# Performance work log

Measured on AMD Instinct MI355X. Metric: run time of the kernel, lower is better.

## Reference

```python
import jax, jax.numpy as jnp
import numpy as np

NUM_NODES = 262144        # 1024 graphs x 256 nodes
NODES_PER_GRAPH = 256
NUM_GRAPHS = NUM_NODES // NODES_PER_GRAPH
NUM_EDGES = 2097152       # avg degree 8
NUM_FEATURES = 9
NUM_STATIONS = 8


def setup_inputs() -> dict:
    key = jax.random.key(0)
    ks = jax.random.split(key, 12)
    # edges constrained within each graph so batched-graph semantics hold
    src_local = jax.random.randint(ks[0], (NUM_EDGES,), 0, NODES_PER_GRAPH)
    dst_local = jax.random.randint(ks[1], (NUM_EDGES,), 0, NODES_PER_GRAPH)
    graph_of_edge = jax.random.randint(ks[2], (NUM_EDGES,), 0, NUM_GRAPHS)
    offset = graph_of_edge * NODES_PER_GRAPH
    edge_index = jnp.stack([src_local + offset, dst_local + offset]).astype(jnp.int64)
    station_ids = jnp.array([0, 37, 73, 110, 146, 183, 219, 255], dtype=jnp.int64)
    s = lambda k, shape, fan_in: jax.random.normal(k, shape, jnp.float32) / np.sqrt(fan_in)
    return {
        "x": jax.random.normal(ks[3], (NUM_NODES, NUM_FEATURES), jnp.float32),
        "edge_index": edge_index,
        "station_ids": station_ids,
        "W1": s(ks[4], (NUM_FEATURES, 32), NUM_FEATURES),
        "b1": jnp.zeros((32,), jnp.float32),
        "W2": s(ks[5], (32, 64), 32),
        "b2": jnp.zeros((64,), jnp.float32),
        "fc1_W": s(ks[6], (128, 64), 128),
        "fc1_b": jnp.zeros((64,), jnp.float32),
        "fc2_W": s(ks[7], (64, 1), 64),
        "fc2_b": jnp.zeros((1,), jnp.float32),
    }


def _gcn_conv(x, W, b, src, dst, n_nodes):
    """PyG GCNConv: add self-loops, symmetric normalization, linear first."""
    h = x @ W                                              # [N, C_out]
    # degree includes the self-loop (+1), counted on target nodes
    deg = jnp.zeros((n_nodes,), h.dtype).at[dst].add(1.0) + 1.0
    dinv = jax.lax.rsqrt(deg)                              # deg >= 1, safe
    norm = dinv[src] * dinv[dst]                           # [E]
    out = jnp.zeros_like(h).at[dst].add(norm[:, None] * h[src])
    out = out + (dinv * dinv)[:, None] * h                 # self-loop term
    return out + b


def reference(x, edge_index, station_ids, W1, b1, W2, b2, fc1_W, fc1_b, fc2_W, fc2_b):
    n = x.shape[0]
    src, dst = edge_index[0], edge_index[1]
    h = jax.nn.relu(_gcn_conv(x, W1, b1, src, dst, n))     # [N, 32]
    h = jax.nn.relu(_gcn_conv(h, W2, b2, src, dst, n))     # [N, 64]
    # global mean pool per graph (batch = node_idx // NODES_PER_GRAPH)
    batch = jnp.arange(n) // NODES_PER_GRAPH
    sums = jax.ops.segment_sum(h, batch, num_segments=NUM_GRAPHS)
    counts = jax.ops.segment_sum(jnp.ones((n,), h.dtype), batch, num_segments=NUM_GRAPHS)
    global_ctx = sums / counts[:, None]                    # [B, 64]
    # per-station gather-MLP, vectorized over stations
    idx = jnp.arange(NUM_GRAPHS)[:, None] * NODES_PER_GRAPH + station_ids[None, :]  # [B, S]
    station_emb = h[idx]                                   # [B, S, 64]
    ctx = jnp.broadcast_to(global_ctx[:, None, :], station_emb.shape)
    combined = jnp.concatenate([station_emb, ctx], axis=-1)  # [B, S, 128]
    q = jax.nn.relu(combined @ fc1_W + fc1_b) @ fc2_W + fc2_b  # [B, S, 1]
    return q[..., 0]                                       # [B, S]
```

## Files before the change

kernel.cpp:

```cpp
#include <hip/hip_runtime.h>
#include <hip/hip_bf16.h>


#define NNODES 262144
#define NPG 256
#define NGRAPHS 1024
#define NEDGES 2097152
#define NFEAT 9
#define ECAP2 2560
#define T_EDGES 8192
#define NTILES (NEDGES / T_EDGES)
#define TPB 512
#define NBLK 256

typedef __hip_bfloat16 bf16;
typedef short short8 __attribute__((ext_vector_type(8)));
typedef float f32x4 __attribute__((ext_vector_type(4)));

__device__ __forceinline__ float bfbits(unsigned short u) { return __uint_as_float(((unsigned)u) << 16); }
__device__ __forceinline__ unsigned short f2bbits(float v) { bf16 b = __float2bfloat16(v); return *(unsigned short*)&b; }


__global__ void __launch_bounds__(1024) k_gsort(const int* __restrict__ src,
                                                const int* __restrict__ dst,
                                                int* __restrict__ gcur,
                                                unsigned short* __restrict__ gout) {
    __shared__ unsigned short edg[T_EDGES];
    __shared__ unsigned short pay[T_EDGES];
    __shared__ int cnt[NGRAPHS];
    __shared__ int goff[NGRAPHS];
    int t = threadIdx.x;
    int base = blockIdx.x * T_EDGES;
    cnt[t] = 0;
    __syncthreads();
    const int4* s4 = (const int4*)(src + base);
    const int4* d4 = (const int4*)(dst + base);
#pragma unroll
    for (int k = 0; k < T_EDGES / 4096; ++k) {
        int idx = k * 1024 + t;
        int4 dv = d4[idx];
        int4 sv = s4[idx];
        int i0 = idx * 4;
        edg[i0]     = (unsigned short)(dv.x >> 8);
        edg[i0 + 1] = (unsigned short)(dv.y >> 8);
        edg[i0 + 2] = (unsigned short)(dv.z >> 8);
        edg[i0 + 3] = (unsigned short)(dv.w >> 8);
        pay[i0]     = (unsigned short)(((dv.x & 255) << 8) | (sv.x & 255));
        pay[i0 + 1] = (unsigned short)(((dv.y & 255) << 8) | (sv.y & 255));
        pay[i0 + 2] = (unsigned short)(((dv.z & 255) << 8) | (sv.z & 255));
        pay[i0 + 3] = (unsigned short)(((dv.w & 255) << 8) | (sv.w & 255));
        atomicAdd(&cnt[dv.x >> 8], 1);
        atomicAdd(&cnt[dv.y >> 8], 1);
        atomicAdd(&cnt[dv.z >> 8], 1);
        atomicAdd(&cnt[dv.w >> 8], 1);
    }
    __syncthreads();
    {
        int c = cnt[t];
        goff[t] = c ? atomicAdd(&gcur[t * 16], c) : 0;
        cnt[t] = 0;
    }
    __syncthreads();
#pragma unroll
    for (int k = 0; k < T_EDGES / 1024; ++k) {
        int i = k * 1024 + t;
        int g = edg[i];
        int pos = atomicAdd(&cnt[g], 1);
        int off = goff[g] + pos;
        if (off < ECAP2) gout[(size_t)g * ECAP2 + off] = pay[i];
    }
}


__global__ void __launch_bounds__(TPB) k_fused(
    const float* __restrict__ x, const int* __restrict__ station_ids,
    const float* __restrict__ W1, const float* __restrict__ b1,
    const float* __restrict__ W2, const float* __restrict__ b2,
    const float* __restrict__ fc1W, const float* __restrict__ fc1b,
    const float* __restrict__ fc2W, const float* __restrict__ fc2b,
    const int* __restrict__ gcnt, const unsigned short* __restrict__ gedges,
    float* __restrict__ out) {

    __shared__ __align__(16) unsigned char Ms[65536];
    __shared__ __align__(16) unsigned char BufA[17024];
    __shared__ __align__(16) unsigned char BufB[17024];
    __shared__ __align__(16) unsigned char BufC[19456];
    __shared__ __align__(16) unsigned short fc1s16[8192];
    __shared__ __align__(16) unsigned short W2Ts[64 * 40];
    __shared__ float W1s[288];
    __shared__ float dinvs[256];
    __shared__ unsigned short Rl[260];
    __shared__ unsigned char El[ECAP2];
    __shared__ unsigned int sru[512];
    __shared__ float sts[512];
    __shared__ float meanf[64];
    __shared__ float poolf[64];
    __shared__ unsigned char stmap[256];
    __shared__ float b1s[32], b2s[64], fc1bs[64], fc2ws[64];
    __shared__ int stids[8];
    __shared__ float fc2bv;

    int t = threadIdx.x;
    int lane = t & 63, wvid = t >> 6;
    int m = lane & 15, quad = lane >> 4;

    float* xsf = (float*)BufC;
    unsigned short* EPa = (unsigned short*)(BufC + 9216);
    unsigned short* G1T = (unsigned short*)BufA;
    unsigned short* H1T = (unsigned short*)BufB;
    unsigned short* S2 = (unsigned short*)BufC;

    for (int i = t; i < NFEAT * 32; i += TPB) W1s[i] = W1[i];
    for (int i = t; i < 2048; i += TPB)
        W2Ts[(i >> 5) * 40 + (i & 31)] = f2bbits(W2[(i & 31) * 64 + (i >> 5)]);
    for (int i = t; i < 8192; i += TPB) fc1s16[i] = f2bbits(fc1W[i]);
    if (t < 32) b1s[t] = b1[t];
    if (t < 64) { b2s[t] = b2[t]; fc1bs[t] = fc1b[t]; fc2ws[t] = fc2W[t]; }
    if (t < 8) stids[t] = station_ids[t];
    if (t == 0) fc2bv = fc2b[0];
    if (t < 256) stmap[t] = 255;
    __syncthreads();
    if (t < 8) stmap[stids[t] & 255] = (unsigned char)t;

    for (int g = blockIdx.x; g < NGRAPHS; g += NBLK) {
        int nbase = g * NPG;

        int ecnt = min(gcnt[g * 16], ECAP2);
        {
            const uint4* gev = (const uint4*)(gedges + (size_t)g * ECAP2);
            uint4* epv = (uint4*)EPa;
            for (int i = t; i < ECAP2 / 8; i += TPB) epv[i] = gev[i];
        }
        const float* xg = x + (size_t)nbase * NFEAT;
        for (int i = t; i < NPG * NFEAT; i += TPB) xsf[i] = xg[i];
        if (t < 64) poolf[t] = 0.f;
        if (t < 256) sru[t] = 0u;
        {
            uint4* mz = (uint4*)Ms;
            uint4 z = {0u, 0u, 0u, 0u};
            for (int i = t; i < 4096; i += TPB) mz[i] = z;
        }
        __syncthreads();

        for (int i = t; i < ecnt; i += TPB) atomicAdd(&sru[EPa[i] >> 8], 1u);
        __syncthreads();

        if (wvid == 0) {
            int b0 = sru[lane * 4], b1v = sru[lane * 4 + 1], b2v = sru[lane * 4 + 2], b3 = sru[lane * 4 + 3];
            int s = b0 + b1v + b2v + b3;
            int inc = s;
            for (int off = 1; off < 64; off <<= 1) {
                int y = __shfl_up(inc, off);
                if (lane >= off) inc += y;
            }
            int run = inc - s;
            Rl[lane * 4] = (unsigned short)run; sru[256 + lane * 4] = run;
            dinvs[lane * 4] = rsqrtf((float)(b0 + 1)); run += b0;
            Rl[lane * 4 + 1] = (unsigned short)run; sru[257 + lane * 4] = run;
            dinvs[lane * 4 + 1] = rsqrtf((float)(b1v + 1)); run += b1v;
            Rl[lane * 4 + 2] = (unsigned short)run; sru[258 + lane * 4] = run;
            dinvs[lane * 4 + 2] = rsqrtf((float)(b2v + 1)); run += b2v;
            Rl[lane * 4 + 3] = (unsigned short)run; sru[259 + lane * 4] = run;
            dinvs[lane * 4 + 3] = rsqrtf((float)(b3 + 1));
            if (lane == 63) Rl[256] = (unsigned short)inc;
        }
        __syncthreads();

        for (int i = t; i < ecnt; i += TPB) {
            unsigned short v = EPa[i];
            unsigned p = atomicAdd(&sru[256 + (v >> 8)], 1u);
            if (p < ECAP2) El[p] = (unsigned char)(v & 255);
        }
        __syncthreads();

        if (t < 256) {
            int dl = t >> 1, q = t & 1;
            int d = dl;
            float did = dinvs[d];
            if ((d >> 7) == q)
                *(unsigned short*)(Ms + dl * 512 + (((d >> 3) ^ (d & 15)) * 16) + (d & 7) * 2)
                    = f2bbits(did * did);
            int r0 = Rl[d], r1 = Rl[d + 1];
            for (int e = r0; e < r1; ++e) {
                int s = El[e];
                if ((s >> 7) == q) {
                    unsigned short* p =
                        (unsigned short*)(Ms + dl * 512 + (((s >> 3) ^ (d & 15)) * 16) + (s & 7) * 2);
                    *p = f2bbits(bfbits(*p) + did * dinvs[s]);
                }
            }
        } else {
            int n = t - 256;
            float xv[NFEAT];
#pragma unroll
            for (int k = 0; k < NFEAT; k++) xv[k] = xsf[n * NFEAT + k];
#pragma unroll 4
            for (int c = 0; c < 32; c++) {
                float acc = 0.f;
#pragma unroll
                for (int k = 0; k < NFEAT; k++) acc += xv[k] * W1s[k * 32 + c];
                G1T[c * 266 + n] = f2bbits(acc);
            }
        }
        __syncthreads();

        {
            f32x4 acc[2] = {};
            for (int kt = 0; kt < 8; ++kt) {
                short8 af = *(const short8*)(Ms + (wvid * 16 + m) * 512 + (((kt * 4 + quad) ^ m) * 16));
                short8 bf0 = *(const short8*)(BufA + (size_t)m * 532 + kt * 64 + quad * 16);
                short8 bf1 = *(const short8*)(BufA + (size_t)(16 + m) * 532 + kt * 64 + quad * 16);
                acc[0] = __builtin_amdgcn_mfma_f32_16x16x32_bf16(af, bf0, acc[0], 0, 0, 0);
                acc[1] = __builtin_amdgcn_mfma_f32_16x16x32_bf16(af, bf1, acc[1], 0, 0, 0);
            }
#pragma unroll
            for (int ni = 0; ni < 2; ++ni) {
                int ch = ni * 16 + m;
                float bb = b1s[ch];
#pragma unroll
                for (int r = 0; r < 4; ++r) {
                    int node = wvid * 16 + quad * 4 + r;
                    H1T[ch * 266 + node] = f2bbits(fmaxf(acc[ni][r] + bb, 0.f));
                }
            }
        }
        __syncthreads();

        {
            uint4* mz = (uint4*)Ms;
            uint4 z = {0u, 0u, 0u, 0u};
            for (int i = t; i < 4096; i += TPB) mz[i] = z;
        }
        __syncthreads();
        {
            int dl = t >> 2, q = t & 3;
            int d = 128 + dl;
            float did = dinvs[d];
            if (((d & 255) >> 6) == q) {
                int sd = d & 255;
                *(unsigned short*)(Ms + dl * 512 + (((sd >> 3) ^ (d & 15)) * 16) + (sd & 7) * 2)
                    = f2bbits(did * did);
            }
            int r0 = Rl[d], r1 = Rl[d + 1];
            for (int e = r0; e < r1; ++e) {
                int s = El[e];
                if ((s >> 6) == q) {
                    unsigned short* p =
                        (unsigned short*)(Ms + dl * 512 + (((s >> 3) ^ (d & 15)) * 16) + (s & 7) * 2);
                    *p = f2bbits(bfbits(*p) + did * dinvs[s]);
                }
            }
        }
        __syncthreads();

        {
            f32x4 acc[2] = {};
            for (int kt = 0; kt < 8; ++kt) {
                short8 af = *(const short8*)(Ms + (wvid * 16 + m) * 512 + (((kt * 4 + quad) ^ m) * 16));
                short8 bf0 = *(const short8*)(BufA + (size_t)m * 532 + kt * 64 + quad * 16);
                short8 bf1 = *(const short8*)(BufA + (size_t)(16 + m) * 532 + kt * 64 + quad * 16);
                acc[0] = __builtin_amdgcn_mfma_f32_16x16x32_bf16(af, bf0, acc[0], 0, 0, 0);
                acc[1] = __builtin_amdgcn_mfma_f32_16x16x32_bf16(af, bf1, acc[1], 0, 0, 0);
            }
#pragma unroll
            for (int ni = 0; ni < 2; ++ni) {
                int ch = ni * 16 + m;
                float bb = b1s[ch];
#pragma unroll
                for (int r = 0; r < 4; ++r) {
                    int node = 128 + wvid * 16 + quad * 4 + r;
                    H1T[ch * 266 + node] = f2bbits(fmaxf(acc[ni][r] + bb, 0.f));
                }
            }
        }
        __syncthreads();

        {
            f32x4 acc[2] = {};
            for (int kt = 0; kt < 8; ++kt) {
                short8 af = *(const short8*)(Ms + (wvid * 16 + m) * 512 + (((kt * 4 + quad) ^ m) * 16));
                short8 bf0 = *(const short8*)(BufB + (size_t)m * 532 + kt * 64 + quad * 16);
                short8 bf1 = *(const short8*)(BufB + (size_t)(16 + m) * 532 + kt * 64 + quad * 16);
                acc[0] = __builtin_amdgcn_mfma_f32_16x16x32_bf16(af, bf0, acc[0], 0, 0, 0);
                acc[1] = __builtin_amdgcn_mfma_f32_16x16x32_bf16(af, bf1, acc[1], 0, 0, 0);
            }
#pragma unroll
            for (int ni = 0; ni < 2; ++ni) {
                int ch = ni * 16 + m;
#pragma unroll
                for (int r = 0; r < 4; ++r) {
                    int node = 128 + wvid * 16 + quad * 4 + r;
                    S2[node * 38 + ch] = f2bbits(acc[ni][r]);
                }
            }
        }
        __syncthreads();

        {
            uint4* mz = (uint4*)Ms;
            uint4 z = {0u, 0u, 0u, 0u};
            for (int i = t; i < 4096; i += TPB) mz[i] = z;
        }
        __syncthreads();
        {
            int dl = t >> 2, q = t & 3;
            int d = dl;
            float did = dinvs[d];
            if ((d >> 6) == q)
                *(unsigned short*)(Ms + dl * 512 + (((d >> 3) ^ (d & 15)) * 16) + (d & 7) * 2)
                    = f2bbits(did * did);
            int r0 = Rl[d], r1 = Rl[d + 1];
            for (int e = r0; e < r1; ++e) {
                int s = El[e];
                if ((s >> 6) == q) {
                    unsigned short* p =
                        (unsigned short*)(Ms + dl * 512 + (((s >> 3) ^ (d & 15)) * 16) + (s & 7) * 2);
                    *p = f2bbits(bfbits(*p) + did * dinvs[s]);
                }
            }
        }
        __syncthreads();

        {
            f32x4 acc[2] = {};
            for (int kt = 0; kt < 8; ++kt) {
                short8 af = *(const short8*)(Ms + (wvid * 16 + m) * 512 + (((kt * 4 + quad) ^ m) * 16));
                short8 bf0 = *(const short8*)(BufB + (size_t)m * 532 + kt * 64 + quad * 16);
                short8 bf1 = *(const short8*)(BufB + (size_t)(16 + m) * 532 + kt * 64 + quad * 16);
                acc[0] = __builtin_amdgcn_mfma_f32_16x16x32_bf16(af, bf0, acc[0], 0, 0, 0);
                acc[1] = __builtin_amdgcn_mfma_f32_16x16x32_bf16(af, bf1, acc[1], 0, 0, 0);
            }
#pragma unroll
            for (int ni = 0; ni < 2; ++ni) {
                int ch = ni * 16 + m;
#pragma unroll
                for (int r = 0; r < 4; ++r) {
                    int node = wvid * 16 + quad * 4 + r;
                    S2[node * 38 + ch] = f2bbits(acc[ni][r]);
                }
            }
        }
        __syncthreads();

        {
#pragma unroll
            for (int mi = 0; mi < 2; ++mi) {
                int mt = wvid * 2 + mi;
                short8 af = *(const short8*)(BufC + (size_t)(mt * 16 + m) * 76 + quad * 16);
#pragma unroll
                for (int ni = 0; ni < 4; ++ni) {
                    short8 bf = *(const short8*)((const unsigned char*)W2Ts + (size_t)(ni * 16 + m) * 80 + quad * 16);
                    f32x4 c = {};
                    c = __builtin_amdgcn_mfma_f32_16x16x32_bf16(af, bf, c, 0, 0, 0);
                    int ch = ni * 16 + m;
                    float bb = b2s[ch];
                    float hv[4];
                    float p = 0.f;
#pragma unroll
                    for (int r = 0; r < 4; ++r) { hv[r] = fmaxf(c[r] + bb, 0.f); p += hv[r]; }
                    p += __shfl_down(p, 32);
                    p += __shfl_down(p, 16);
                    if (quad == 0) atomicAdd(&poolf[ch], p);
#pragma unroll
                    for (int r = 0; r < 4; ++r) {
                        int node = mt * 16 + quad * 4 + r;
                        int si = stmap[node];
                        if (si != 255) sts[si * 64 + ch] = hv[r];
                    }
                }
            }
        }
        __syncthreads();

        if (t < 64) meanf[t] = poolf[t] * (1.0f / 256.0f);
        __syncthreads();

        {
            int l = lane;
            int si = wvid;
            const float* st = sts + si * 64;
            float acc = 0.f;
#pragma unroll 8
            for (int k = 0; k < 64; k++) acc += st[k] * bfbits(fc1s16[k * 64 + l]);
#pragma unroll 8
            for (int k = 0; k < 64; k++) acc += meanf[k] * bfbits(fc1s16[(64 + k) * 64 + l]);
            float a = fmaxf(acc + fc1bs[l], 0.f) * fc2ws[l];
            for (int off = 32; off > 0; off >>= 1) a += __shfl_down(a, off);
            if (l == 0) out[g * 8 + si] = a + fc2bv;
        }
        __syncthreads();
    }
}


extern "C" void kernel_launch(void* const* d_in, const int* in_sizes, int n_in,
                              void* d_out, int out_size, void* d_ws, size_t ws_size,
                              hipStream_t stream) {
    const float* x = (const float*)d_in[0];
    const int* ei = (const int*)d_in[1];
    const int* station_ids = (const int*)d_in[2];
    const float* W1 = (const float*)d_in[3];
    const float* b1 = (const float*)d_in[4];
    const float* W2 = (const float*)d_in[5];
    const float* bias2 = (const float*)d_in[6];
    const float* fc1W = (const float*)d_in[7];
    const float* fc1b = (const float*)d_in[8];
    const float* fc2W = (const float*)d_in[9];
    const float* fc2b = (const float*)d_in[10];
    float* out = (float*)d_out;
    (void)in_sizes; (void)n_in; (void)out_size; (void)ws_size;

    char* ws = (char*)d_ws;
    int* gcur = (int*)ws;
    unsigned short* gout = (unsigned short*)(ws + 0x10000);

    const int* esrc = ei;
    const int* edst = ei + NEDGES;

    hipMemsetAsync(gcur, 0, NGRAPHS * 16 * sizeof(int), stream);
    k_gsort<<<NTILES, 1024, 0, stream>>>(esrc, edst, gcur, gout);
    k_fused<<<NBLK, TPB, 0, stream>>>(x, station_ids, W1, b1, W2, bias2,
                                      fc1W, fc1b, fc2W, fc2b, gcur, gout, out);
}
```

Before: 200.0 us.

## Replace atomic graph-bucket sort with histogram, scan and scatter passes

The single-pass edge bucketing kernel, which reserved per-graph output ranges with global atomics on a memset counter array, is split into three kernels. A per-tile histogram kernel writes counts, a scan kernel computes exclusive per-tile offsets and the per-graph totals, and a scatter kernel places edges using only shared-memory atomics. This removes the memset and the contended global atomics and makes edge placement deterministic. In exchange it adds two kernel launches and reads the destination array twice.

```diff
diff --git a/kernel.cpp b/kernel.cpp
--- a/kernel.cpp
+++ b/kernel.cpp
@@ -21,18 +21,57 @@
 __device__ __forceinline__ unsigned short f2bbits(float v) { bf16 b = __float2bfloat16(v); return *(unsigned short*)&b; }
 
 
-__global__ void __launch_bounds__(1024) k_gsort(const int* __restrict__ src,
-                                                const int* __restrict__ dst,
-                                                int* __restrict__ gcur,
-                                                unsigned short* __restrict__ gout) {
+__global__ void __launch_bounds__(1024) k_hist(const int* __restrict__ dst,
+                                               int* __restrict__ hist) {
+    __shared__ int cnt[NGRAPHS];
+    int t = threadIdx.x;
+    cnt[t] = 0;
+    __syncthreads();
+    const int4* d4 = (const int4*)(dst + blockIdx.x * T_EDGES);
+#pragma unroll
+    for (int k = 0; k < T_EDGES / 4096; ++k) {
+        int4 dv = d4[k * 1024 + t];
+        atomicAdd(&cnt[dv.x >> 8], 1);
+        atomicAdd(&cnt[dv.y >> 8], 1);
+        atomicAdd(&cnt[dv.z >> 8], 1);
+        atomicAdd(&cnt[dv.w >> 8], 1);
+    }
+    __syncthreads();
+    hist[blockIdx.x * NGRAPHS + t] = cnt[t];
+}
+
+__global__ void __launch_bounds__(256) k_scan(int* __restrict__ hist,
+                                              int* __restrict__ gcnt) {
+    __shared__ int wsum[4];
+    int g = blockIdx.x;
+    int t = threadIdx.x;
+    int lane = t & 63, wv = t >> 6;
+    int v = hist[t * NGRAPHS + g];
+    int inc = v;
+    for (int off = 1; off < 64; off <<= 1) {
+        int y = __shfl_up(inc, off);
+        if (lane >= off) inc += y;
+    }
+    if (lane == 63) wsum[wv] = inc;
+    __syncthreads();
+    int wpre = 0;
+#pragma unroll
+    for (int w = 0; w < 3; ++w) if (w < wv) wpre += wsum[w];
+    int exc = wpre + inc - v;
+    hist[t * NGRAPHS + g] = exc;
+    if (t == 255) gcnt[g * 16] = exc + v;
+}
+
+__global__ void __launch_bounds__(1024) k_scatter(const int* __restrict__ src,
+                                                  const int* __restrict__ dst,
+                                                  const int* __restrict__ hist,
+                                                  unsigned short* __restrict__ gout) {
     __shared__ unsigned short edg[T_EDGES];
     __shared__ unsigned short pay[T_EDGES];
-    __shared__ int cnt[NGRAPHS];
-    __shared__ int goff[NGRAPHS];
+    __shared__ int cur[NGRAPHS];
     int t = threadIdx.x;
     int base = blockIdx.x * T_EDGES;
-    cnt[t] = 0;
-    __syncthreads();
+    cur[t] = hist[blockIdx.x * NGRAPHS + t];
     const int4* s4 = (const int4*)(src + base);
     const int4* d4 = (const int4*)(dst + base);
 #pragma unroll
@@ -49,24 +88,13 @@
         pay[i0 + 1] = (unsigned short)(((dv.y & 255) << 8) | (sv.y & 255));
         pay[i0 + 2] = (unsigned short)(((dv.z & 255) << 8) | (sv.z & 255));
         pay[i0 + 3] = (unsigned short)(((dv.w & 255) << 8) | (sv.w & 255));
-        atomicAdd(&cnt[dv.x >> 8], 1);
-        atomicAdd(&cnt[dv.y >> 8], 1);
-        atomicAdd(&cnt[dv.z >> 8], 1);
-        atomicAdd(&cnt[dv.w >> 8], 1);
-    }
-    __syncthreads();
-    {
-        int c = cnt[t];
-        goff[t] = c ? atomicAdd(&gcur[t * 16], c) : 0;
-        cnt[t] = 0;
     }
     __syncthreads();
 #pragma unroll
     for (int k = 0; k < T_EDGES / 1024; ++k) {
         int i = k * 1024 + t;
         int g = edg[i];
-        int pos = atomicAdd(&cnt[g], 1);
-        int off = goff[g] + pos;
+        int off = atomicAdd(&cur[g], 1);
         if (off < ECAP2) gout[(size_t)g * ECAP2 + off] = pay[i];
     }
 }
@@ -411,14 +439,16 @@
     (void)in_sizes; (void)n_in; (void)out_size; (void)ws_size;
 
     char* ws = (char*)d_ws;
-    int* gcur = (int*)ws;
+    int* gcnt = (int*)ws;
     unsigned short* gout = (unsigned short*)(ws + 0x10000);
+    int* hist = (int*)(ws + 0x510000);
 
     const int* esrc = ei;
     const int* edst = ei + NEDGES;
 
-    hipMemsetAsync(gcur, 0, NGRAPHS * 16 * sizeof(int), stream);
-    k_gsort<<<NTILES, 1024, 0, stream>>>(esrc, edst, gcur, gout);
+    k_hist<<<NTILES, 1024, 0, stream>>>(edst, hist);
+    k_scan<<<NGRAPHS, 256, 0, stream>>>(hist, gcnt);
+    k_scatter<<<NTILES, 1024, 0, stream>>>(esrc, edst, hist, gout);
     k_fused<<<NBLK, TPB, 0, stream>>>(x, station_ids, W1, b1, W2, bias2,
-                                      fc1W, fc1b, fc2W, fc2b, gcur, gout, out);
+                                      fc1W, fc1b, fc2W, fc2b, gcnt, gout, out);
 }
```

Measured after the change: 200.8 us. No clear change (+0.4%).
